# Optimization experiments

Measured on AMD Instinct MI355X. Metric: run time of the kernel, lower is better.

Reference implementation:

```python
import jax, jax.numpy as jnp
import numpy as np

B_SCALE = 1.3195079565048218  # per_level_scale
N_LEVELS = 4                  # kernel hardcodes 4 levels
F = 4                         # kernel hardcodes 4 features per level
BASE = 32.0                   # kernel hardcodes base resolution 32
MAX_PARAMS = 2 ** 19
N_POINTS = 2097152


def _level_meta():
    offsets = []
    off = 0
    for i in range(N_LEVELS):
        res = int(np.ceil(BASE * np.exp(i * np.log(B_SCALE)) - 1.0)) + 1
        p = res ** 3
        p = p if p % 8 == 0 else ((p + 7) // 8) * 8
        p = min(MAX_PARAMS, p)
        offsets.append(off)
        off += p
    return offsets, off

OFFSETS, TOTAL_PARAMS = _level_meta()
TOTAL_HASH_SIZE = TOTAL_PARAMS * F  # 2772480


def setup_inputs() -> dict:
    key = jax.random.key(0)
    k1, k2 = jax.random.split(key)
    # scale to [0, 0.9) so all 8 corner indices stay inside each level's grid
    positions = jax.random.uniform(k1, (N_POINTS, 3), dtype=jnp.float32) * 0.9
    # original init: uniform(-1e-4, 1e-4); small random values
    table = jax.random.normal(k2, (TOTAL_HASH_SIZE,), dtype=jnp.float32) * 1e-4
    return {"positions": positions, "table": table}


def _encode(positions, table):
    tab = table.reshape(-1, F)  # [total_params, 4]
    n = positions.shape[0]
    outs = []
    for level in range(N_LEVELS):
        scale = BASE * (B_SCALE ** level) - 1.0
        res = int(np.ceil(scale)) + 1
        pos = positions * scale + 0.5            # [n,3]
        grid = jnp.floor(pos)
        frac = pos - grid                         # trilinear fractions
        grid = grid.astype(jnp.int32)
        acc = jnp.zeros((n, F), positions.dtype)
        for c in range(8):  # 8 corners of the cell
            w = jnp.ones((n,), positions.dtype)
            idx = jnp.zeros((n,), jnp.int32)
            stride = 1
            for d in range(3):
                if (c >> d) & 1:
                    coord = grid[:, d] + 1
                    w = w * frac[:, d]
                else:
                    coord = grid[:, d]
                    w = w * (1.0 - frac[:, d])
                idx = idx + coord * stride
                stride *= res
            acc = acc + w[:, None] * tab[OFFSETS[level] + idx]
        outs.append(acc)
    return jnp.concatenate(outs, axis=1)  # [n, 16]


def reference(positions, table):
    return _encode(positions, table)
```

## Files before the change

### kernel.cpp

```cpp
#include <hip/hip_runtime.h>
#include <math.h>


#define NBINS        512
#define BIN_SCALE    (8.0f / 0.9f)
#define SCAT_THREADS 512
#define PTS_PER_BLK  4096
#define SCAT_ITERS   (PTS_PER_BLK / SCAT_THREADS)
#define PTS_PER_PASS (SCAT_THREADS * 4)
#define NPASS        (PTS_PER_BLK / PTS_PER_PASS)
#define CAP          4608

#define ENC_THREADS  1024

#define D0 6
#define D1 7
#define D2 9
#define D3 11
#define A0 0
#define A1 (A0 + D0*D0*D0)
#define A2 (A1 + D1*D1*D1)
#define A3 (A2 + D2*D2*D2)
#define LDS_TOT (A3 + D3*D3*D3)

typedef float vfloat4 __attribute__((ext_vector_type(4)));

__device__ __forceinline__ int bin_of(float x, float y, float z) {
    int bx = (int)(x * BIN_SCALE); bx = bx < 0 ? 0 : (bx > 7 ? 7 : bx);
    int by = (int)(y * BIN_SCALE); by = by < 0 ? 0 : (by > 7 ? 7 : by);
    int bz = (int)(z * BIN_SCALE); bz = bz < 0 ? 0 : (bz > 7 ? 7 : bz);
    return bx | (by << 3) | (bz << 6);
}


__global__ __launch_bounds__(SCAT_THREADS) void scatter_cap_kernel(
    const float* __restrict__ pos, int n, int* __restrict__ cursor,
    float4* __restrict__ sorted, int bin_stride)
{
    __shared__ float4         lds_rec[PTS_PER_BLK];
    __shared__ unsigned short lds_bin[PTS_PER_BLK];
    __shared__ int lds_hist[NBINS];
    __shared__ int lds_lbase[NBINS];
    __shared__ int lds_gbase[NBINS];
    __shared__ int lds_wsum[8];

    int tid = threadIdx.x;
    long base = (long)blockIdx.x * PTS_PER_BLK;
    lds_hist[tid] = 0;
    __syncthreads();

    float px[4 * NPASS], py[4 * NPASS], pz[4 * NPASS];
    int br[4 * NPASS];
#pragma unroll
    for (int pass = 0; pass < NPASS; ++pass) {
        long p0 = base + (long)pass * PTS_PER_PASS + 4 * tid;
        int ii = pass * 4;
        if (p0 + 4 <= n) {
            const float4* v = (const float4*)(pos + 3 * p0);
            float4 A = v[0], B = v[1], C = v[2];
            px[ii+0]=A.x; py[ii+0]=A.y; pz[ii+0]=A.z;
            px[ii+1]=A.w; py[ii+1]=B.x; pz[ii+1]=B.y;
            px[ii+2]=B.z; py[ii+2]=B.w; pz[ii+2]=C.x;
            px[ii+3]=C.y; py[ii+3]=C.z; pz[ii+3]=C.w;
#pragma unroll
            for (int q = 0; q < 4; ++q) {
                int b = bin_of(px[ii+q], py[ii+q], pz[ii+q]);
                int r = atomicAdd(&lds_hist[b], 1);
                br[ii+q] = (r << 9) | b;
            }
        } else {
#pragma unroll
            for (int q = 0; q < 4; ++q) {
                long p = p0 + q;
                int packed = -1;
                if (p < n) {
                    float x = pos[3*p], y = pos[3*p+1], z = pos[3*p+2];
                    px[ii+q]=x; py[ii+q]=y; pz[ii+q]=z;
                    int b = bin_of(x, y, z);
                    int r = atomicAdd(&lds_hist[b], 1);
                    packed = (r << 9) | b;
                }
                br[ii+q] = packed;
            }
        }
    }
    __syncthreads();

    int lane = tid & 63, wid = tid >> 6;
    int cntb = lds_hist[tid];
    int v = cntb;
#pragma unroll
    for (int off = 1; off < 64; off <<= 1) {
        int u = __shfl_up(v, off, 64);
        if (lane >= off) v += u;
    }
    if (lane == 63) lds_wsum[wid] = v;
    __syncthreads();
    if (tid < 8) {
        int w = lds_wsum[tid];
#pragma unroll
        for (int off = 1; off < 8; off <<= 1) {
            int u = __shfl_up(w, off, 8);
            if (tid >= off) w += u;
        }
        lds_wsum[tid] = w;
    }
    if (cntb) lds_gbase[tid] = atomicAdd(&cursor[tid], cntb);
    __syncthreads();
    int wbase = wid ? lds_wsum[wid - 1] : 0;
    int excl  = wbase + v - cntb;
    lds_lbase[tid] = excl;
    __syncthreads();

#pragma unroll
    for (int ii = 0; ii < 4 * NPASS; ++ii) {
        if (br[ii] < 0) continue;
        int b = br[ii] & (NBINS - 1);
        int r = br[ii] >> 9;
        int s = lds_lbase[b] + r;
        long p = base + (long)(ii >> 2) * PTS_PER_PASS + 4 * tid + (ii & 3);
        lds_rec[s] = make_float4(px[ii], py[ii], pz[ii], __int_as_float((int)p));
        lds_bin[s] = (unsigned short)b;
    }
    __syncthreads();

    long rem = (long)n - base;
    int tot = rem >= PTS_PER_BLK ? PTS_PER_BLK : (rem > 0 ? (int)rem : 0);
    for (int s = tid; s < tot; s += SCAT_THREADS) {
        float4 rec = lds_rec[s];
        int b = lds_bin[s];
        int off_in_bin = s - lds_lbase[b];
        long slot = (long)b * bin_stride + lds_gbase[b] + off_in_bin;
        sorted[slot] = rec;
    }
}

template<int D>
__device__ __forceinline__ void stage_win(
    float4* __restrict__ dst, const float4* __restrict__ tab,
    int off, int res, int Bx, int By, int Bz, int tid)
{
    const int DD = D * D, DDD = D * D * D;
    for (int e = tid; e < DDD; e += ENC_THREADS) {
        int iz  = e / DD;
        int rem = e - iz * DD;
        int iy  = rem / D;
        int ix  = rem - iy * D;
        int gx = Bx + ix; gx = gx < 0 ? 0 : (gx > res - 1 ? res - 1 : gx);
        int gy = By + iy; gy = gy < 0 ? 0 : (gy > res - 1 ? res - 1 : gy);
        int gz = Bz + iz; gz = gz < 0 ? 0 : (gz > res - 1 ? res - 1 : gz);
        dst[e] = tab[off + gx + gy * res + gz * res * res];
    }
}

template<int D>
__device__ __forceinline__ float4 interp_one(
    const float4* __restrict__ lds, const float4* __restrict__ tab,
    float x, float y, float z, float scale, int res, int off,
    int Bx, int By, int Bz)
{
    float hx = x * scale + 0.5f, hy = y * scale + 0.5f, hz = z * scale + 0.5f;
    float fx = floorf(hx), fy = floorf(hy), fz = floorf(hz);
    float wx = hx - fx, wy = hy - fy, wz = hz - fz;
    float ox = 1.0f - wx, oy = 1.0f - wy, oz = 1.0f - wz;
    int gx = (int)fx, gy = (int)fy, gz = (int)fz;
    int lx = gx - Bx, ly = gy - By, lz = gz - Bz;
    float4 acc = make_float4(0.f, 0.f, 0.f, 0.f);
    if ((unsigned)lx <= (unsigned)(D - 2) &&
        (unsigned)ly <= (unsigned)(D - 2) &&
        (unsigned)lz <= (unsigned)(D - 2)) {
        int basei = (lz * D + ly) * D + lx;
#pragma unroll
        for (int c = 0; c < 8; ++c) {
            int   idx = basei + ((c & 1) ? 1 : 0) + ((c & 2) ? D : 0) + ((c & 4) ? D * D : 0);
            float w   = ((c & 1) ? wx : ox) * ((c & 2) ? wy : oy) * ((c & 4) ? wz : oz);
            float4 v  = lds[idx];
            acc.x += w * v.x; acc.y += w * v.y; acc.z += w * v.z; acc.w += w * v.w;
        }
    } else {
        int res2  = res * res;
        int basei = off + gx + gy * res + gz * res2;
#pragma unroll
        for (int c = 0; c < 8; ++c) {
            int   idx = basei + ((c & 1) ? 1 : 0) + ((c & 2) ? res : 0) + ((c & 4) ? res2 : 0);
            float w   = ((c & 1) ? wx : ox) * ((c & 2) ? wy : oy) * ((c & 4) ? wz : oz);
            float4 v  = tab[idx];
            acc.x += w * v.x; acc.y += w * v.y; acc.z += w * v.z; acc.w += w * v.w;
        }
    }
    return acc;
}

__global__ __launch_bounds__(ENC_THREADS) void encode_bin_kernel(
    const float4* __restrict__ sorted,
    const int* __restrict__ cursor,
    const float4* __restrict__ tab,
    float4* __restrict__ out,
    float s0, float s1, float s2, float s3,
    int r0, int r1, int r2, int r3,
    int o0, int o1, int o2, int o3)
{
    __shared__ float4 lds[LDS_TOT];

    int nb = (int)gridDim.x;
    int b  = (int)blockIdx.x;
    b = (b & 7) * (nb >> 3) + (b >> 3);

    int cnt = cursor[b];
    int tid = threadIdx.x;

    int bx = b & 7, by = (b >> 3) & 7, bz = b >> 6;
    float lox = bx * 0.1125f, loy = by * 0.1125f, loz = bz * 0.1125f;

    int B0x = (int)floorf(lox * s0 + 0.5f), B0y = (int)floorf(loy * s0 + 0.5f), B0z = (int)floorf(loz * s0 + 0.5f);
    int B1x = (int)floorf(lox * s1 + 0.5f), B1y = (int)floorf(loy * s1 + 0.5f), B1z = (int)floorf(loz * s1 + 0.5f);
    int B2x = (int)floorf(lox * s2 + 0.5f), B2y = (int)floorf(loy * s2 + 0.5f), B2z = (int)floorf(loz * s2 + 0.5f);
    int B3x = (int)floorf(lox * s3 + 0.5f), B3y = (int)floorf(loy * s3 + 0.5f), B3z = (int)floorf(loz * s3 + 0.5f);

    stage_win<D0>(lds + A0, tab, o0, r0, B0x, B0y, B0z, tid);
    stage_win<D1>(lds + A1, tab, o1, r1, B1x, B1y, B1z, tid);
    stage_win<D2>(lds + A2, tab, o2, r2, B2x, B2y, B2z, tid);
    stage_win<D3>(lds + A3, tab, o3, r3, B3x, B3y, B3z, tid);
    __syncthreads();

    if (cnt == 0) return;

    int iters = (cnt + ENC_THREADS - 1) / ENC_THREADS;
    const float4* sbin = sorted + (long)b * CAP;
    int jmax = CAP - 1;

    int local = tid;
    vfloat4 rv = __builtin_nontemporal_load(
        (const vfloat4*)&sbin[local <= jmax ? local : jmax]);

    for (int it = 0; it < iters; ++it) {
        int nloc = local + ENC_THREADS;
        vfloat4 nx = rv;
        if (it + 1 < iters)
            nx = __builtin_nontemporal_load(
                (const vfloat4*)&sbin[nloc <= jmax ? nloc : jmax]);
        if (local < cnt) {
            float x = rv.x, y = rv.y, z = rv.z;
            int p = __float_as_int(rv.w);
            float4* op = out + (long)p * 4;
            float4 a0 = interp_one<D0>(lds + A0, tab, x, y, z, s0, r0, o0, B0x, B0y, B0z);
            float4 a1 = interp_one<D1>(lds + A1, tab, x, y, z, s1, r1, o1, B1x, B1y, B1z);
            float4 a2 = interp_one<D2>(lds + A2, tab, x, y, z, s2, r2, o2, B2x, B2y, B2z);
            float4 a3 = interp_one<D3>(lds + A3, tab, x, y, z, s3, r3, o3, B3x, B3y, B3z);
            op[0] = a0; op[1] = a1; op[2] = a2; op[3] = a3;
        }
        rv = nx;
        local = nloc;
    }
}


__device__ __forceinline__ void interp_levels(
    float4 rec, const float4* __restrict__ tab, float4* __restrict__ o,
    float s0, float s1, float s2, float s3,
    int r0, int r1, int r2, int r3,
    int o0, int o1, int o2, int o3)
{
    float scales[4] = { s0, s1, s2, s3 };
    int   ress[4]   = { r0, r1, r2, r3 };
    int   offs[4]   = { o0, o1, o2, o3 };
#pragma unroll
    for (int l = 0; l < 4; ++l) {
        float scale = scales[l];
        int   res   = ress[l];
        int   off   = offs[l];
        float hx = rec.x * scale + 0.5f;
        float hy = rec.y * scale + 0.5f;
        float hz = rec.z * scale + 0.5f;
        float gx = floorf(hx), gy = floorf(hy), gz = floorf(hz);
        float wx = hx - gx,   wy = hy - gy,   wz = hz - gz;
        float ox = 1.0f - wx, oy = 1.0f - wy, oz = 1.0f - wz;
        int res2 = res * res;
        int base = off + (int)gx + (int)gy * res + (int)gz * res2;
        float4 acc = make_float4(0.f, 0.f, 0.f, 0.f);
#pragma unroll
        for (int c = 0; c < 8; ++c) {
            int   idx = base + ((c & 1) ? 1 : 0) + ((c & 2) ? res : 0) + ((c & 4) ? res2 : 0);
            float w   = ((c & 1) ? wx : ox) * ((c & 2) ? wy : oy) * ((c & 4) ? wz : oz);
            float4 v  = tab[idx];
            acc.x += w * v.x; acc.y += w * v.y; acc.z += w * v.z; acc.w += w * v.w;
        }
        o[l] = acc;
    }
}


__global__ __launch_bounds__(SCAT_THREADS) void hist_kernel(
    const float* __restrict__ pos, int n, int* __restrict__ hist)
{
    __shared__ int lh[NBINS];
    int tid = threadIdx.x;
    lh[tid] = 0;
    __syncthreads();
    long base = (long)blockIdx.x * PTS_PER_BLK;
#pragma unroll
    for (int j = 0; j < SCAT_ITERS; ++j) {
        long p = base + j * SCAT_THREADS + tid;
        if (p < n) {
            float x = pos[3 * p], y = pos[3 * p + 1], z = pos[3 * p + 2];
            atomicAdd(&lh[bin_of(x, y, z)], 1);
        }
    }
    __syncthreads();
    int c = lh[tid];
    if (c) atomicAdd(&hist[tid], c);
}

__global__ __launch_bounds__(256) void scan_kernel(
    const int* __restrict__ hist, int* __restrict__ cursor)
{
    __shared__ int partials[256];
    int t = threadIdx.x;
    int a = hist[2 * t], b = hist[2 * t + 1];
    int sum = a + b;
    partials[t] = sum;
    __syncthreads();
    for (int off = 1; off < 256; off <<= 1) {
        int v = (t >= off) ? partials[t - off] : 0;
        __syncthreads();
        partials[t] += v;
        __syncthreads();
    }
    int base = partials[t] - sum;
    cursor[2 * t]     = base;
    cursor[2 * t + 1] = base + a;
}

__global__ __launch_bounds__(256) void encode_kernel(
    const float4* __restrict__ sorted, const float4* __restrict__ tab,
    float4* __restrict__ out, int n,
    float s0, float s1, float s2, float s3,
    int r0, int r1, int r2, int r3,
    int o0, int o1, int o2, int o3)
{
    int j = blockIdx.x * blockDim.x + threadIdx.x;
    if (j >= n) return;
    vfloat4 rv = __builtin_nontemporal_load((const vfloat4*)&sorted[j]);
    float4 rec = make_float4(rv.x, rv.y, rv.z, rv.w);
    int p = __float_as_int(rec.w);
    interp_levels(rec, tab, out + (long)p * 4,
                  s0, s1, s2, s3, r0, r1, r2, r3, o0, o1, o2, o3);
}

__global__ __launch_bounds__(256) void encode_direct_kernel(
    const float* __restrict__ pos, const float4* __restrict__ tab,
    float4* __restrict__ out, int n_points,
    float s0, float s1, float s2, float s3,
    int r0, int r1, int r2, int r3,
    int o0, int o1, int o2, int o3)
{
    int t = blockIdx.x * blockDim.x + threadIdx.x;
    int p = t >> 2;
    if (p >= n_points) return;
    int l = t & 3;
    float scale = (l == 0) ? s0 : (l == 1) ? s1 : (l == 2) ? s2 : s3;
    int   res   = (l == 0) ? r0 : (l == 1) ? r1 : (l == 2) ? r2 : r3;
    int   off   = (l == 0) ? o0 : (l == 1) ? o1 : (l == 2) ? o2 : o3;
    float px = pos[3 * p], py = pos[3 * p + 1], pz = pos[3 * p + 2];
    float hx = px * scale + 0.5f, hy = py * scale + 0.5f, hz = pz * scale + 0.5f;
    float gx = floorf(hx), gy = floorf(hy), gz = floorf(hz);
    float wx = hx - gx, wy = hy - gy, wz = hz - gz;
    float ox = 1.f - wx, oy = 1.f - wy, oz = 1.f - wz;
    int res2 = res * res;
    int base = off + (int)gx + (int)gy * res + (int)gz * res2;
    float4 acc = make_float4(0.f, 0.f, 0.f, 0.f);
#pragma unroll
    for (int c = 0; c < 8; ++c) {
        int   idx = base + ((c & 1) ? 1 : 0) + ((c & 2) ? res : 0) + ((c & 4) ? res2 : 0);
        float w   = ((c & 1) ? wx : ox) * ((c & 2) ? wy : oy) * ((c & 4) ? wz : oz);
        float4 v  = tab[idx];
        acc.x += w * v.x; acc.y += w * v.y; acc.z += w * v.z; acc.w += w * v.w;
    }
    out[t] = acc;
}

extern "C" void kernel_launch(void* const* d_in, const int* in_sizes, int n_in,
                              void* d_out, int out_size, void* d_ws, size_t ws_size,
                              hipStream_t stream) {
    const float*  positions = (const float*)d_in[0];
    const float4* table     = (const float4*)d_in[1];
    float4*       out       = (float4*)d_out;
    int n = in_sizes[0] / 3;

    const double B_SCALE = 1.3195079565048218;
    const double BASE = 32.0;
    const long   MAX_PARAMS = 1L << 19;
    float scales[4]; int res[4], offs[4];
    long off = 0;
    for (int l = 0; l < 4; ++l) {
        double s = BASE * pow(B_SCALE, (double)l) - 1.0;
        scales[l] = (float)s;
        int r = (int)ceil(s) + 1;
        res[l] = r;
        offs[l] = (int)off;
        long pcount = (long)r * r * r;
        if (pcount % 8 != 0) pcount = (pcount + 7) / 8 * 8;
        if (pcount > MAX_PARAMS) pcount = MAX_PARAMS;
        off += pcount;
    }

    size_t need_cap   = (size_t)NBINS * sizeof(int) + (size_t)NBINS * CAP * 16;
    size_t need_exact = (size_t)NBINS * sizeof(int) * 2 + (size_t)n * 16;

    if (ws_size >= need_cap && n <= NBINS * (CAP - 512)) {
        int*    cursor = (int*)d_ws;
        float4* sorted = (float4*)(cursor + NBINS);

        int grid_pts = (n + PTS_PER_BLK - 1) / PTS_PER_BLK;

        (void)hipMemsetAsync(cursor, 0, NBINS * sizeof(int), stream);
        scatter_cap_kernel<<<grid_pts, SCAT_THREADS, 0, stream>>>(
            positions, n, cursor, sorted, CAP);
        encode_bin_kernel<<<NBINS, ENC_THREADS, 0, stream>>>(
            sorted, cursor, table, out,
            scales[0], scales[1], scales[2], scales[3],
            res[0], res[1], res[2], res[3],
            offs[0], offs[1], offs[2], offs[3]);
    } else if (ws_size >= need_exact) {
        int*    hist   = (int*)d_ws;
        int*    cursor = hist + NBINS;
        float4* sorted = (float4*)(cursor + NBINS);

        int grid_pts = (n + PTS_PER_BLK - 1) / PTS_PER_BLK;
        int grid_enc = (n + 255) / 256;

        (void)hipMemsetAsync(hist, 0, NBINS * sizeof(int), stream);
        hist_kernel<<<grid_pts, SCAT_THREADS, 0, stream>>>(positions, n, hist);
        scan_kernel<<<1, 256, 0, stream>>>(hist, cursor);
        scatter_cap_kernel<<<grid_pts, SCAT_THREADS, 0, stream>>>(
            positions, n, cursor, sorted, 0);
        encode_kernel<<<grid_enc, 256, 0, stream>>>(
            sorted, table, out, n,
            scales[0], scales[1], scales[2], scales[3],
            res[0], res[1], res[2], res[3],
            offs[0], offs[1], offs[2], offs[3]);
    } else {
        long n_threads = 4L * n;
        long grid = (n_threads + 255) / 256;
        encode_direct_kernel<<<dim3((unsigned)grid), dim3(256), 0, stream>>>(
            positions, table, out, n,
            scales[0], scales[1], scales[2], scales[3],
            res[0], res[1], res[2], res[3],
            offs[0], offs[1], offs[2], offs[3]);
    }
}
```

Baseline: 223.4 us.

## Halve scatter block size and recompute bin instead of storing it in LDS

The scatter kernel now processes 2048 points per block instead of 4096, so each thread handles a single pass of four points, and the per-record LDS bin array is removed. The bin is recomputed from coordinates during the global write-out. This cuts LDS use per block, which can raise occupancy, and lowers register pressure. In exchange it launches twice as many blocks, doubling the global cursor atomics and giving shorter contiguous runs per bin in the sorted output.

Result: slower. 233.0 us (+4.3%).

```diff
diff --git a/kernel.cpp b/kernel.cpp
--- a/kernel.cpp
+++ b/kernel.cpp
@@ -5,10 +5,8 @@
 #define NBINS        512
 #define BIN_SCALE    (8.0f / 0.9f)
 #define SCAT_THREADS 512
-#define PTS_PER_BLK  4096
+#define PTS_PER_BLK  2048
 #define SCAT_ITERS   (PTS_PER_BLK / SCAT_THREADS)
-#define PTS_PER_PASS (SCAT_THREADS * 4)
-#define NPASS        (PTS_PER_BLK / PTS_PER_PASS)
 #define CAP          4608
 
 #define ENC_THREADS  1024
@@ -37,8 +35,7 @@
     const float* __restrict__ pos, int n, int* __restrict__ cursor,
     float4* __restrict__ sorted, int bin_stride)
 {
-    __shared__ float4         lds_rec[PTS_PER_BLK];
-    __shared__ unsigned short lds_bin[PTS_PER_BLK];
+    __shared__ float4 lds_rec[PTS_PER_BLK];
     __shared__ int lds_hist[NBINS];
     __shared__ int lds_lbase[NBINS];
     __shared__ int lds_gbase[NBINS];
@@ -49,24 +46,22 @@
     lds_hist[tid] = 0;
     __syncthreads();
 
-    float px[4 * NPASS], py[4 * NPASS], pz[4 * NPASS];
-    int br[4 * NPASS];
-#pragma unroll
-    for (int pass = 0; pass < NPASS; ++pass) {
-        long p0 = base + (long)pass * PTS_PER_PASS + 4 * tid;
-        int ii = pass * 4;
+    float px[4], py[4], pz[4];
+    int br[4];
+    {
+        long p0 = base + 4 * tid;
         if (p0 + 4 <= n) {
             const float4* v = (const float4*)(pos + 3 * p0);
             float4 A = v[0], B = v[1], C = v[2];
-            px[ii+0]=A.x; py[ii+0]=A.y; pz[ii+0]=A.z;
-            px[ii+1]=A.w; py[ii+1]=B.x; pz[ii+1]=B.y;
-            px[ii+2]=B.z; py[ii+2]=B.w; pz[ii+2]=C.x;
-            px[ii+3]=C.y; py[ii+3]=C.z; pz[ii+3]=C.w;
+            px[0]=A.x; py[0]=A.y; pz[0]=A.z;
+            px[1]=A.w; py[1]=B.x; pz[1]=B.y;
+            px[2]=B.z; py[2]=B.w; pz[2]=C.x;
+            px[3]=C.y; py[3]=C.z; pz[3]=C.w;
 #pragma unroll
             for (int q = 0; q < 4; ++q) {
-                int b = bin_of(px[ii+q], py[ii+q], pz[ii+q]);
+                int b = bin_of(px[q], py[q], pz[q]);
                 int r = atomicAdd(&lds_hist[b], 1);
-                br[ii+q] = (r << 9) | b;
+                br[q] = (r << 9) | b;
             }
         } else {
 #pragma unroll
@@ -75,12 +70,12 @@
                 int packed = -1;
                 if (p < n) {
                     float x = pos[3*p], y = pos[3*p+1], z = pos[3*p+2];
-                    px[ii+q]=x; py[ii+q]=y; pz[ii+q]=z;
+                    px[q]=x; py[q]=y; pz[q]=z;
                     int b = bin_of(x, y, z);
                     int r = atomicAdd(&lds_hist[b], 1);
                     packed = (r << 9) | b;
                 }
-                br[ii+q] = packed;
+                br[q] = packed;
             }
         }
     }
@@ -113,14 +108,13 @@
     __syncthreads();
 
 #pragma unroll
-    for (int ii = 0; ii < 4 * NPASS; ++ii) {
-        if (br[ii] < 0) continue;
-        int b = br[ii] & (NBINS - 1);
-        int r = br[ii] >> 9;
+    for (int q = 0; q < 4; ++q) {
+        if (br[q] < 0) continue;
+        int b = br[q] & (NBINS - 1);
+        int r = br[q] >> 9;
         int s = lds_lbase[b] + r;
-        long p = base + (long)(ii >> 2) * PTS_PER_PASS + 4 * tid + (ii & 3);
-        lds_rec[s] = make_float4(px[ii], py[ii], pz[ii], __int_as_float((int)p));
-        lds_bin[s] = (unsigned short)b;
+        long p = base + 4 * tid + q;
+        lds_rec[s] = make_float4(px[q], py[q], pz[q], __int_as_float((int)p));
     }
     __syncthreads();
 
@@ -128,7 +122,7 @@
     int tot = rem >= PTS_PER_BLK ? PTS_PER_BLK : (rem > 0 ? (int)rem : 0);
     for (int s = tid; s < tot; s += SCAT_THREADS) {
         float4 rec = lds_rec[s];
-        int b = lds_bin[s];
+        int b = bin_of(rec.x, rec.y, rec.z);
         int off_in_bin = s - lds_lbase[b];
         long slot = (long)b * bin_stride + lds_gbase[b] + off_in_bin;
         sorted[slot] = rec;
```
